# Kernel tuning notes

Hardware: AMD Instinct MI355X
Metric: run time of the kernel (lower is better)

Reference implementation:

```python
import jax, jax.numpy as jnp
import numpy as np

B, L, DM = 4, 1024, 1024
DI = int(2.0 * DM)            # d_inner = ssm_ratio * d_model
N = 16                        # d_state
R = int(np.ceil(DM / 16))     # dt_rank = 64
DT_MIN, DT_MAX = 1e-3, 1e-1


def setup_inputs() -> dict:
    key = jax.random.key(0)
    ks = jax.random.split(key, 8)
    s = 0.02
    # dt_proj bias init: inverse-softplus of log-uniform dt in [dt_min, dt_max]
    dt = jnp.exp(jax.random.uniform(ks[5], (DI,)) * (np.log(DT_MAX) - np.log(DT_MIN)) + np.log(DT_MIN))
    dt_bias = dt + jnp.log(-jnp.expm1(-dt))
    # A_log init: log(1..N) tiled per channel (S4D-real init)
    A_logs = jnp.log(jnp.tile(jnp.arange(1, N + 1, dtype=jnp.float32), (DI, 1)))
    return {
        "x": jax.random.normal(ks[0], (B, L, DM), jnp.float32),
        "W_in": jax.random.normal(ks[1], (DM, 2 * DI), jnp.float32) * s,
        "conv_w": jax.random.normal(ks[2], (DI, 1, 3), jnp.float32) * 0.1,
        "conv_b": jnp.zeros((DI,), jnp.float32),
        "W_x": jax.random.normal(ks[3], (DI, R + 2 * N), jnp.float32) * s,
        "W_dt": jax.random.normal(ks[4], (R, DI), jnp.float32) * (R ** -0.5),
        "dt_bias": dt_bias.astype(jnp.float32),
        "A_logs": A_logs,
        "Ds": jnp.ones((DI,), jnp.float32),
        "ln_g": jnp.ones((DI,), jnp.float32),
        "ln_b": jnp.zeros((DI,), jnp.float32),
        "W_out": jax.random.normal(ks[6], (DI, DM), jnp.float32) * s,
        "b_out": jnp.zeros((DM,), jnp.float32),
    }


def reference(x, W_in, conv_w, conv_b, W_x, W_dt, dt_bias, A_logs, Ds, ln_g, ln_b, W_out, b_out):
    di, n = Ds.shape[0], A_logs.shape[1]
    r = W_dt.shape[0]
    # in_proj and gate branch
    xz = x @ W_in                                   # (B,L,2*di)
    xi = xz[..., :di]
    z = jax.nn.silu(xz[..., di:])                   # (B,L,di)
    # depthwise conv over sequence dim (kernel 3, pad 1)
    xc = jnp.swapaxes(xi, 1, 2)                     # (B,di,L)
    xc = jax.lax.conv_general_dilated(
        xc, conv_w, (1,), [(1, 1)],
        dimension_numbers=("NCH", "OIH", "NCH"),
        feature_group_count=di) + conv_b[None, :, None]
    u = jax.nn.silu(jnp.swapaxes(xc, 1, 2))         # (B,L,di)
    # input-dependent dt, B, C
    x_dbl = u @ W_x                                 # (B,L,r+2n)
    dts = x_dbl[..., :r] @ W_dt                     # (B,L,di)
    Bs = x_dbl[..., r:r + n]                        # (B,L,n)
    Cs = x_dbl[..., r + n:]                         # (B,L,n)
    delta = jax.nn.softplus(dts + dt_bias)          # (B,L,di)
    A = -jnp.exp(A_logs)                            # (di,n)

    def step(h, inp):
        dt, ut, bt, ct = inp                        # (B,di),(B,di),(B,n),(B,n)
        h = jnp.exp(dt[..., None] * A) * h + (dt * ut)[..., None] * bt[:, None, :]
        return h, jnp.einsum("bdn,bn->bd", h, ct)

    xs = (jnp.swapaxes(delta, 0, 1), jnp.swapaxes(u, 0, 1),
          jnp.swapaxes(Bs, 0, 1), jnp.swapaxes(Cs, 0, 1))
    h0 = jnp.zeros((x.shape[0], di, n), x.dtype)
    _, ys = jax.lax.scan(step, h0, xs)              # (L,B,di)
    y = jnp.swapaxes(ys, 0, 1) + Ds * u             # skip term D*u
    # LayerNorm over channels
    mu = y.mean(-1, keepdims=True)
    var = ((y - mu) ** 2).mean(-1, keepdims=True)
    y = (y - mu) / jnp.sqrt(var + 1e-5) * ln_g + ln_b
    y = y * z                                       # gating
    v = y.mean(axis=1)                              # pool='mean' over D
    return v @ W_out + b_out                        # (B, out_dim)
```

## Files before the change

kernel.cpp:

```cpp
#include <hip/hip_runtime.h>
#include <math.h>

#define B_ 4
#define L_ 1024
#define DM_ 1024
#define DI_ 2048
#define N_ 16
#define R_ 64
#define BT_ (B_*L_)
#define NX_ 96
#define CH_ 16
#define LC_ (L_/CH_)
#define KC_ 8
#define KCL_ (DI_/KC_)

typedef unsigned short u16;
typedef unsigned int u32;
typedef short bf16x8 __attribute__((ext_vector_type(8)));
typedef u16 u16x8 __attribute__((ext_vector_type(8)));
typedef float f32x4 __attribute__((ext_vector_type(4)));

__device__ __forceinline__ float silu_f(float x) { return x / (1.f + expf(-x)); }
__device__ __forceinline__ float softplus_f(float x) {
  return x > 0.f ? x + log1pf(expf(-x)) : log1pf(expf(x));
}
__device__ __forceinline__ u16 bf16_rne(float f) {
  u32 u = __float_as_uint(f);
  u32 r = (u + 0x7FFFu + ((u >> 16) & 1u)) >> 16;
  return (u16)r;
}
__device__ __forceinline__ float bf16_to_f(u16 h) {
  return __uint_as_float(((u32)h) << 16);
}
__device__ __forceinline__ void gload_lds16(const void* g, void* l) {
  __builtin_amdgcn_global_load_lds((const __attribute__((address_space(1))) void*)g,
                                   (__attribute__((address_space(3))) void*)l, 16, 0, 0);
}

#define SWZ16(r, s) ((r) * 64 + ((((s) ^ (((r) >> 1) & 3))) << 4))

__global__ __launch_bounds__(256) void wsplit_kernel(const float* __restrict__ W,
                                                     u16* __restrict__ Th,
                                                     u16* __restrict__ Tl) {
  __shared__ float tile[32][33];
  const int n0 = blockIdx.x * 32;
  const int k0 = blockIdx.y * 32;
  const int t = threadIdx.x;
  {
    int kr = t >> 3, nc = (t & 7) * 4;
    float4 v = *(const float4*)&W[(size_t)(k0 + kr) * (2 * DI_) + n0 + nc];
    tile[kr][nc + 0] = v.x; tile[kr][nc + 1] = v.y;
    tile[kr][nc + 2] = v.z; tile[kr][nc + 3] = v.w;
  }
  __syncthreads();
  {
    int nr = t >> 3, kc = (t & 7) * 4;
    u16 h[4], l[4];
#pragma unroll
    for (int i = 0; i < 4; ++i) {
      float f = tile[kc + i][nr];
      h[i] = bf16_rne(f);
      l[i] = bf16_rne(f - bf16_to_f(h[i]));
    }
    size_t o = (size_t)(n0 + nr) * DM_ + k0 + kc;
    *(ushort4*)&Th[o] = make_ushort4(h[0], h[1], h[2], h[3]);
    *(ushort4*)&Tl[o] = make_ushort4(l[0], l[1], l[2], l[3]);
  }
}

__global__ __launch_bounds__(256) void xsplit_kernel(const float* __restrict__ x,
                                                     u16* __restrict__ xh,
                                                     u16* __restrict__ xl) {
  int gid = blockIdx.x * 256 + threadIdx.x;
  float4 v = *(const float4*)&x[(size_t)gid * 4];
  ushort4 h, l;
  h.x = bf16_rne(v.x); l.x = bf16_rne(v.x - bf16_to_f(h.x));
  h.y = bf16_rne(v.y); l.y = bf16_rne(v.y - bf16_to_f(h.y));
  h.z = bf16_rne(v.z); l.z = bf16_rne(v.z - bf16_to_f(h.z));
  h.w = bf16_rne(v.w); l.w = bf16_rne(v.w - bf16_to_f(h.w));
  *(ushort4*)&xh[(size_t)gid * 4] = h;
  *(ushort4*)&xl[(size_t)gid * 4] = l;
}

__global__ __launch_bounds__(512) void gemm1_mfma(const u16* __restrict__ Xh,
                                                  const u16* __restrict__ Xl,
                                                  const u16* __restrict__ Bh,
                                                  const u16* __restrict__ Bl,
                                                  float* __restrict__ xi,
                                                  float* __restrict__ z) {
  __shared__ __align__(16) char lds[49152];

  const int tid = threadIdx.x;
  const int m0 = blockIdx.x * 128;
  const int n0 = blockIdx.y * 256;
  const int wv = tid >> 6;
  const int lane = tid & 63;
  const int wr = wv >> 2, wc = wv & 3;
  const int lrow = lane & 15, lk = lane >> 4;

  const u16* gbase[6];
  int ldsO[6];
  size_t goff[6];
#pragma unroll
  for (int i = 0; i < 6; ++i) {
    int c = wv * 6 + i;
    int O = c << 10;
    int to;
    const u16* gb;
    if (O < 8192)       { gb = Xh + (size_t)m0 * DM_; to = O; }
    else if (O < 16384) { gb = Xl + (size_t)m0 * DM_; to = O - 8192; }
    else if (O < 32768) { gb = Bh + (size_t)n0 * DM_; to = O - 16384; }
    else                { gb = Bl + (size_t)n0 * DM_; to = O - 32768; }
    int r = (to >> 6) + (lane >> 2);
    int s_src = (lane & 3) ^ ((r >> 1) & 3);
    gbase[i] = gb;
    ldsO[i] = O;
    goff[i] = (size_t)r * DM_ + s_src * 8;
  }

  f32x4 acc[4][4];
#pragma unroll
  for (int i = 0; i < 4; ++i)
#pragma unroll
    for (int j = 0; j < 4; ++j) acc[i][j] = (f32x4){0.f, 0.f, 0.f, 0.f};

  for (int kk = 0; kk < DM_ / 32; ++kk) {
    const int k0 = kk * 32;
#pragma unroll
    for (int i = 0; i < 6; ++i) {
      gload_lds16(gbase[i] + goff[i] + k0, lds + ldsO[i]);
    }
    __syncthreads();

    bf16x8 a_h[4], a_l[4], b_h[4], b_l[4];
#pragma unroll
    for (int mi = 0; mi < 4; ++mi) {
      int r = wr * 64 + mi * 16 + lrow;
      a_h[mi] = *(const bf16x8*)(lds + SWZ16(r, lk));
      a_l[mi] = *(const bf16x8*)(lds + 8192 + SWZ16(r, lk));
    }
#pragma unroll
    for (int ni = 0; ni < 4; ++ni) {
      int r = wc * 64 + ni * 16 + lrow;
      b_h[ni] = *(const bf16x8*)(lds + 16384 + SWZ16(r, lk));
      b_l[ni] = *(const bf16x8*)(lds + 32768 + SWZ16(r, lk));
    }
#pragma unroll
    for (int mi = 0; mi < 4; ++mi)
#pragma unroll
      for (int ni = 0; ni < 4; ++ni) {
        acc[mi][ni] = __builtin_amdgcn_mfma_f32_16x16x32_bf16(a_h[mi], b_h[ni], acc[mi][ni], 0, 0, 0);
        acc[mi][ni] = __builtin_amdgcn_mfma_f32_16x16x32_bf16(a_h[mi], b_l[ni], acc[mi][ni], 0, 0, 0);
        acc[mi][ni] = __builtin_amdgcn_mfma_f32_16x16x32_bf16(a_l[mi], b_h[ni], acc[mi][ni], 0, 0, 0);
      }
    __syncthreads();
  }

  const bool is_z = (n0 >= DI_);
#pragma unroll
  for (int mi = 0; mi < 4; ++mi) {
#pragma unroll
    for (int ni = 0; ni < 4; ++ni) {
      int mrow = m0 + wr * 64 + mi * 16 + (lane >> 4) * 4;
      int ncol = n0 + wc * 64 + ni * 16 + (lane & 15);
#pragma unroll
      for (int rg = 0; rg < 4; ++rg) {
        float v = acc[mi][ni][rg];
        int m = mrow + rg;
        if (!is_z) {
          xi[(size_t)m * DI_ + ncol] = v;
        } else {
          z[(size_t)m * DI_ + (ncol - DI_)] = silu_f(v);
        }
      }
    }
  }
}

__global__ __launch_bounds__(256) void conv_silu_kernel(const float* __restrict__ xi,
                                                        const float* __restrict__ cw,
                                                        const float* __restrict__ cb,
                                                        float* __restrict__ u) {
  int gid = blockIdx.x * 256 + threadIdx.x;
  int idx = gid * 4;
  int d = idx & (DI_ - 1);
  int t = (idx >> 11) & (L_ - 1);
  float4 xc = *(const float4*)&xi[idx];
  float4 xm = make_float4(0.f, 0.f, 0.f, 0.f);
  float4 xp = make_float4(0.f, 0.f, 0.f, 0.f);
  if (t > 0) xm = *(const float4*)&xi[idx - DI_];
  if (t < L_ - 1) xp = *(const float4*)&xi[idx + DI_];
  float4 o;
  {
    float w0 = cw[(d + 0) * 3], w1 = cw[(d + 0) * 3 + 1], w2 = cw[(d + 0) * 3 + 2];
    o.x = silu_f(cb[d + 0] + w0 * xm.x + w1 * xc.x + w2 * xp.x);
  }
  {
    float w0 = cw[(d + 1) * 3], w1 = cw[(d + 1) * 3 + 1], w2 = cw[(d + 1) * 3 + 2];
    o.y = silu_f(cb[d + 1] + w0 * xm.y + w1 * xc.y + w2 * xp.y);
  }
  {
    float w0 = cw[(d + 2) * 3], w1 = cw[(d + 2) * 3 + 1], w2 = cw[(d + 2) * 3 + 2];
    o.z = silu_f(cb[d + 2] + w0 * xm.z + w1 * xc.z + w2 * xp.z);
  }
  {
    float w0 = cw[(d + 3) * 3], w1 = cw[(d + 3) * 3 + 1], w2 = cw[(d + 3) * 3 + 2];
    o.w = silu_f(cb[d + 3] + w0 * xm.w + w1 * xc.w + w2 * xp.w);
  }
  *(float4*)&u[idx] = o;
}

__global__ __launch_bounds__(256) void wxsplit_kernel(const float* __restrict__ Wx,
                                                      u16* __restrict__ Th,
                                                      u16* __restrict__ Tl) {
  int gid = blockIdx.x * 256 + threadIdx.x;
  int n = gid >> 11;
  int k = gid & (DI_ - 1);
  float f = Wx[(size_t)k * NX_ + n];
  u16 h = bf16_rne(f);
  Th[gid] = h;
  Tl[gid] = bf16_rne(f - bf16_to_f(h));
}

__global__ __launch_bounds__(256) void xdbl_mfma(const float* __restrict__ U,
                                                 const u16* __restrict__ Wh,
                                                 const u16* __restrict__ Wl,
                                                 float* __restrict__ Pt) {
  __shared__ u16 Uh_s[128 * 32];
  __shared__ u16 Ul_s[128 * 32];
  __shared__ u16 Wh_s[96 * 32];
  __shared__ u16 Wl_s[96 * 32];

  const int tid = threadIdx.x;
  const int m0 = blockIdx.x * 128;
  const int kc = blockIdx.y;
  const int wv = tid >> 6;
  const int lane = tid & 63;
  const int lrow = lane & 15, lk = lane >> 4;
  const int ra = tid >> 1;
  const int hf = tid & 1;

  f32x4 acc[2][6];
#pragma unroll
  for (int i = 0; i < 2; ++i)
#pragma unroll
    for (int j = 0; j < 6; ++j) acc[i][j] = (f32x4){0.f, 0.f, 0.f, 0.f};

  float af[16];
  uint4 wh_r[3], wl_r[3];
  int wc_row[3], wc_slot[3], wc_buf[3];

  {
    int k0 = kc * KCL_;
    const float* up = &U[(size_t)(m0 + ra) * DI_ + k0 + hf * 16];
    float4 a0 = *(const float4*)(up + 0);
    float4 a1 = *(const float4*)(up + 4);
    float4 a2 = *(const float4*)(up + 8);
    float4 a3 = *(const float4*)(up + 12);
    af[0]=a0.x; af[1]=a0.y; af[2]=a0.z; af[3]=a0.w;
    af[4]=a1.x; af[5]=a1.y; af[6]=a1.z; af[7]=a1.w;
    af[8]=a2.x; af[9]=a2.y; af[10]=a2.z; af[11]=a2.w;
    af[12]=a3.x; af[13]=a3.y; af[14]=a3.z; af[15]=a3.w;
#pragma unroll
    for (int i = 0; i < 3; ++i) {
      int c = tid + 256 * i;
      int buf = c >= 384;
      int cc = c & 383;
      int row = cc >> 2, slot = cc & 3;
      wc_buf[i] = buf; wc_row[i] = row; wc_slot[i] = slot;
      const u16* src = (buf ? Wl : Wh) + (size_t)row * DI_ + k0 + slot * 8;
      uint4 v = *(const uint4*)src;
      if (buf) wl_r[i] = v; else wh_r[i] = v;
    }
  }

  for (int kk = 0; kk < KCL_ / 32; ++kk) {
    __syncthreads();
    {
      u16x8 hv0, hv1, lv0, lv1;
#pragma unroll
      for (int i = 0; i < 8; ++i) {
        u16 h = bf16_rne(af[i]);
        hv0[i] = h;
        lv0[i] = bf16_rne(af[i] - bf16_to_f(h));
      }
#pragma unroll
      for (int i = 0; i < 8; ++i) {
        u16 h = bf16_rne(af[8 + i]);
        hv1[i] = h;
        lv1[i] = bf16_rne(af[8 + i] - bf16_to_f(h));
      }
      int s0 = hf * 2;
      *(u16x8*)((char*)Uh_s + SWZ16(ra, s0)) = hv0;
      *(u16x8*)((char*)Uh_s + SWZ16(ra, s0 + 1)) = hv1;
      *(u16x8*)((char*)Ul_s + SWZ16(ra, s0)) = lv0;
      *(u16x8*)((char*)Ul_s + SWZ16(ra, s0 + 1)) = lv1;
#pragma unroll
      for (int i = 0; i < 3; ++i) {
        char* dst = (char*)(wc_buf[i] ? Wl_s : Wh_s) + SWZ16(wc_row[i], wc_slot[i]);
        *(uint4*)dst = wc_buf[i] ? wl_r[i] : wh_r[i];
      }
    }
    __syncthreads();

    if (kk + 1 < KCL_ / 32) {
      int k0 = kc * KCL_ + (kk + 1) * 32;
      const float* up = &U[(size_t)(m0 + ra) * DI_ + k0 + hf * 16];
      float4 a0 = *(const float4*)(up + 0);
      float4 a1 = *(const float4*)(up + 4);
      float4 a2 = *(const float4*)(up + 8);
      float4 a3 = *(const float4*)(up + 12);
      af[0]=a0.x; af[1]=a0.y; af[2]=a0.z; af[3]=a0.w;
      af[4]=a1.x; af[5]=a1.y; af[6]=a1.z; af[7]=a1.w;
      af[8]=a2.x; af[9]=a2.y; af[10]=a2.z; af[11]=a2.w;
      af[12]=a3.x; af[13]=a3.y; af[14]=a3.z; af[15]=a3.w;
#pragma unroll
      for (int i = 0; i < 3; ++i) {
        const u16* src = (wc_buf[i] ? Wl : Wh) + (size_t)wc_row[i] * DI_ + k0 + wc_slot[i] * 8;
        uint4 v = *(const uint4*)src;
        if (wc_buf[i]) wl_r[i] = v; else wh_r[i] = v;
      }
    }

    bf16x8 a_h[2], a_l[2], b_h[6], b_l[6];
#pragma unroll
    for (int mi = 0; mi < 2; ++mi) {
      int r = wv * 32 + mi * 16 + lrow;
      a_h[mi] = *(const bf16x8*)((const char*)Uh_s + SWZ16(r, lk));
      a_l[mi] = *(const bf16x8*)((const char*)Ul_s + SWZ16(r, lk));
    }
#pragma unroll
    for (int ni = 0; ni < 6; ++ni) {
      int r = ni * 16 + lrow;
      b_h[ni] = *(const bf16x8*)((const char*)Wh_s + SWZ16(r, lk));
      b_l[ni] = *(const bf16x8*)((const char*)Wl_s + SWZ16(r, lk));
    }
#pragma unroll
    for (int mi = 0; mi < 2; ++mi)
#pragma unroll
      for (int ni = 0; ni < 6; ++ni) {
        acc[mi][ni] = __builtin_amdgcn_mfma_f32_16x16x32_bf16(a_h[mi], b_h[ni], acc[mi][ni], 0, 0, 0);
        acc[mi][ni] = __builtin_amdgcn_mfma_f32_16x16x32_bf16(a_h[mi], b_l[ni], acc[mi][ni], 0, 0, 0);
        acc[mi][ni] = __builtin_amdgcn_mfma_f32_16x16x32_bf16(a_l[mi], b_h[ni], acc[mi][ni], 0, 0, 0);
      }
  }

#pragma unroll
  for (int mi = 0; mi < 2; ++mi) {
#pragma unroll
    for (int ni = 0; ni < 6; ++ni) {
      int mrow = m0 + wv * 32 + mi * 16 + (lane >> 4) * 4;
      int ncol = ni * 16 + (lane & 15);
#pragma unroll
      for (int rg = 0; rg < 4; ++rg) {
        Pt[((size_t)kc * BT_ + mrow + rg) * NX_ + ncol] = acc[mi][ni][rg];
      }
    }
  }
}

__global__ __launch_bounds__(256) void xdbl_reduce(const float* __restrict__ Pt,
                                                   float* __restrict__ xdbl) {
  int gid = blockIdx.x * 256 + threadIdx.x;
  float s = 0.f;
#pragma unroll
  for (int kc = 0; kc < KC_; ++kc) s += Pt[(size_t)kc * BT_ * NX_ + gid];
  xdbl[gid] = s;
}

__global__ __launch_bounds__(256) void delta_kernel(const float* __restrict__ xdbl,
                                                    const float* __restrict__ Wdt,
                                                    const float* __restrict__ dtb,
                                                    float* __restrict__ delta) {
  __shared__ float xs[8][R_];
  const int m0 = blockIdx.x * 8;
  const int tid = threadIdx.x;
  for (int i = tid; i < 8 * R_; i += 256) {
    int mi = i >> 6, r = i & 63;
    xs[mi][r] = xdbl[(size_t)(m0 + mi) * NX_ + r];
  }
  __syncthreads();
  float acc[8][8];
#pragma unroll
  for (int mi = 0; mi < 8; ++mi)
#pragma unroll
    for (int j = 0; j < 8; ++j) acc[mi][j] = 0.f;

  for (int r = 0; r < R_; ++r) {
    float wd[8];
#pragma unroll
    for (int j = 0; j < 8; ++j) wd[j] = Wdt[(size_t)r * DI_ + tid + j * 256];
#pragma unroll
    for (int mi = 0; mi < 8; ++mi) {
      float xr = xs[mi][r];
#pragma unroll
      for (int j = 0; j < 8; ++j) acc[mi][j] += xr * wd[j];
    }
  }
#pragma unroll
  for (int j = 0; j < 8; ++j) {
    int d = tid + j * 256;
    float bias = dtb[d];
#pragma unroll
    for (int mi = 0; mi < 8; ++mi) {
      delta[(size_t)(m0 + mi) * DI_ + d] = softplus_f(acc[mi][j] + bias);
    }
  }
}

__global__ __launch_bounds__(256) void scanA_kernel(const float* __restrict__ delta,
                                                    const float* __restrict__ u,
                                                    const float* __restrict__ xdbl,
                                                    const float* __restrict__ A_logs,
                                                    float* __restrict__ P,
                                                    float* __restrict__ Q) {
  const int tid = threadIdx.x;
  const int q = tid & 3;
  const int chan = blockIdx.x * 64 + (tid >> 2);
  const int c = blockIdx.y;
  const int b = chan >> 11;
  const int d = chan & (DI_ - 1);
  float Ac[4];
#pragma unroll
  for (int j = 0; j < 4; ++j) Ac[j] = -expf(A_logs[d * N_ + q * 4 + j]);
  const size_t base = (size_t)b * L_ * DI_ + d;
  const float* xd = xdbl + (size_t)b * L_ * NX_;
  float h[4] = {0.f, 0.f, 0.f, 0.f};
  float pr[4] = {1.f, 1.f, 1.f, 1.f};
  const int t0 = c * LC_;
  for (int tt = 0; tt < LC_; ++tt) {
    int t = t0 + tt;
    float dt = delta[base + (size_t)t * DI_];
    float ut = u[base + (size_t)t * DI_];
    float4 Bt = *(const float4*)&xd[t * NX_ + R_ + q * 4];
    float du = dt * ut;
    float e0 = __expf(dt * Ac[0]), e1 = __expf(dt * Ac[1]);
    float e2 = __expf(dt * Ac[2]), e3 = __expf(dt * Ac[3]);
    h[0] = e0 * h[0] + du * Bt.x; pr[0] *= e0;
    h[1] = e1 * h[1] + du * Bt.y; pr[1] *= e1;
    h[2] = e2 * h[2] + du * Bt.z; pr[2] *= e2;
    h[3] = e3 * h[3] + du * Bt.w; pr[3] *= e3;
  }
  size_t idx = ((size_t)chan * CH_ + c) * N_ + q * 4;
  *(float4*)&P[idx] = make_float4(pr[0], pr[1], pr[2], pr[3]);
  *(float4*)&Q[idx] = make_float4(h[0], h[1], h[2], h[3]);
}

__global__ __launch_bounds__(256) void scanB_kernel(const float* __restrict__ P,
                                                    const float* __restrict__ Q,
                                                    float* __restrict__ H0) {
  int gid = blockIdx.x * 256 + threadIdx.x;
  int chan = gid >> 4;
  int n = gid & 15;
  float h = 0.f;
  for (int c = 0; c < CH_; ++c) {
    size_t idx = ((size_t)chan * CH_ + c) * N_ + n;
    H0[idx] = h;
    h = P[idx] * h + Q[idx];
  }
}

__global__ __launch_bounds__(256) void scanC_kernel(const float* __restrict__ delta,
                                                    float* uy,
                                                    const float* __restrict__ xdbl,
                                                    const float* __restrict__ A_logs,
                                                    const float* __restrict__ Ds,
                                                    const float* __restrict__ H0) {
  const int tid = threadIdx.x;
  const int q = tid & 3;
  const int chan = blockIdx.x * 64 + (tid >> 2);
  const int c = blockIdx.y;
  const int b = chan >> 11;
  const int d = chan & (DI_ - 1);
  float Ac[4];
#pragma unroll
  for (int j = 0; j < 4; ++j) Ac[j] = -expf(A_logs[d * N_ + q * 4 + j]);
  const float Dd = Ds[d];
  const size_t base = (size_t)b * L_ * DI_ + d;
  const float* dl = delta + base;
  float* ul = uy + base;
  const float* xd = xdbl + (size_t)b * L_ * NX_;
  float h[4];
  {
    float4 h0 = *(const float4*)&H0[((size_t)chan * CH_ + c) * N_ + q * 4];
    h[0] = h0.x; h[1] = h0.y; h[2] = h0.z; h[3] = h0.w;
  }
  const int t0 = c * LC_;
  for (int tt = 0; tt < LC_; ++tt) {
    int t = t0 + tt;
    float dt = dl[(size_t)t * DI_];
    float ut = ul[(size_t)t * DI_];
    float4 Bt = *(const float4*)&xd[t * NX_ + R_ + q * 4];
    float4 Ct = *(const float4*)&xd[t * NX_ + R_ + N_ + q * 4];
    float du = dt * ut;
    float e0 = __expf(dt * Ac[0]), e1 = __expf(dt * Ac[1]);
    float e2 = __expf(dt * Ac[2]), e3 = __expf(dt * Ac[3]);
    h[0] = e0 * h[0] + du * Bt.x;
    h[1] = e1 * h[1] + du * Bt.y;
    h[2] = e2 * h[2] + du * Bt.z;
    h[3] = e3 * h[3] + du * Bt.w;
    float p = h[0] * Ct.x + h[1] * Ct.y + h[2] * Ct.z + h[3] * Ct.w;
    p += __shfl_xor(p, 1);
    p += __shfl_xor(p, 2);
    if (q == 0) ul[(size_t)t * DI_] = p + Dd * ut;
  }
}

__global__ __launch_bounds__(256) void stats_kernel(const float* __restrict__ y,
                                                    float* __restrict__ mu,
                                                    float* __restrict__ rs) {
  __shared__ float red[4];
  const int row = blockIdx.x;
  const float* yr = y + (size_t)row * DI_;
  const int tid = threadIdx.x;
  float v[8];
  float s = 0.f;
#pragma unroll
  for (int j = 0; j < 8; ++j) { v[j] = yr[tid + j * 256]; s += v[j]; }
#pragma unroll
  for (int o = 1; o < 64; o <<= 1) s += __shfl_xor(s, o);
  if ((tid & 63) == 0) red[tid >> 6] = s;
  __syncthreads();
  float mu_v = (red[0] + red[1] + red[2] + red[3]) * (1.f / DI_);
  float q = 0.f;
#pragma unroll
  for (int j = 0; j < 8; ++j) { float dd = v[j] - mu_v; q += dd * dd; }
#pragma unroll
  for (int o = 1; o < 64; o <<= 1) q += __shfl_xor(q, o);
  __syncthreads();
  if ((tid & 63) == 0) red[tid >> 6] = q;
  __syncthreads();
  if (tid == 0) {
    float var = (red[0] + red[1] + red[2] + red[3]) * (1.f / DI_);
    mu[row] = mu_v;
    rs[row] = rsqrtf(var + 1e-5f);
  }
}

__global__ __launch_bounds__(256) void vacc_kernel(const float* __restrict__ y,
                                                   const float* __restrict__ z,
                                                   const float* __restrict__ mu,
                                                   const float* __restrict__ rs,
                                                   const float* __restrict__ g,
                                                   const float* __restrict__ bb,
                                                   float* __restrict__ v) {
  const int d = blockIdx.x * 256 + threadIdx.x;
  const int t0 = blockIdx.y * 64;
  const int b = blockIdx.z;
  const float gg = g[d], bbv = bb[d];
  float acc = 0.f;
  for (int tt = 0; tt < 64; ++tt) {
    int row = b * L_ + t0 + tt;
    float yv = y[(size_t)row * DI_ + d];
    float zv = z[(size_t)row * DI_ + d];
    acc += ((yv - mu[row]) * rs[row] * gg + bbv) * zv;
  }
  atomicAdd(&v[b * DI_ + d], acc * (1.f / L_));
}

__global__ __launch_bounds__(256) void outinit_kernel(const float* __restrict__ b_out,
                                                      float* __restrict__ out) {
  int i = blockIdx.x * 256 + threadIdx.x;
  out[i] = b_out[i & (DM_ - 1)];
}

__global__ __launch_bounds__(256) void outgemm_kernel(const float* __restrict__ v,
                                                      const float* __restrict__ Wout,
                                                      float* __restrict__ out) {
  const int m = blockIdx.x * 256 + threadIdx.x;
  const int d0 = blockIdx.y * 128;
  float a0 = 0.f, a1 = 0.f, a2 = 0.f, a3 = 0.f;
  for (int dd = 0; dd < 128; ++dd) {
    float w = Wout[(size_t)(d0 + dd) * DM_ + m];
    a0 += v[0 * DI_ + d0 + dd] * w;
    a1 += v[1 * DI_ + d0 + dd] * w;
    a2 += v[2 * DI_ + d0 + dd] * w;
    a3 += v[3 * DI_ + d0 + dd] * w;
  }
  atomicAdd(&out[0 * DM_ + m], a0);
  atomicAdd(&out[1 * DM_ + m], a1);
  atomicAdd(&out[2 * DM_ + m], a2);
  atomicAdd(&out[3 * DM_ + m], a3);
}

extern "C" void kernel_launch(void* const* d_in, const int* in_sizes, int n_in,
                              void* d_out, int out_size, void* d_ws, size_t ws_size,
                              hipStream_t stream) {
  const float* x      = (const float*)d_in[0];
  const float* W_in   = (const float*)d_in[1];
  const float* conv_w = (const float*)d_in[2];
  const float* conv_b = (const float*)d_in[3];
  const float* W_x    = (const float*)d_in[4];
  const float* W_dt   = (const float*)d_in[5];
  const float* dt_bias= (const float*)d_in[6];
  const float* A_logs = (const float*)d_in[7];
  const float* Ds     = (const float*)d_in[8];
  const float* ln_g   = (const float*)d_in[9];
  const float* ln_b   = (const float*)d_in[10];
  const float* W_out  = (const float*)d_in[11];
  const float* b_out  = (const float*)d_in[12];
  float* out = (float*)d_out;

  float* ws = (float*)d_ws;
  const size_t BIG = (size_t)BT_ * DI_;
  float* xi_buf   = ws;
  float* z_buf    = ws + BIG;
  float* u_buf    = ws + 2 * BIG;
  float* xdbl_buf = ws + 3 * BIG;
  float* mu_buf   = xdbl_buf + (size_t)BT_ * NX_;
  float* rs_buf   = mu_buf + BT_;
  float* v_buf    = rs_buf + BT_;
  float* P_buf    = v_buf + (size_t)B_ * DI_;
  float* Q_buf    = P_buf + (size_t)B_ * DI_ * CH_ * N_;
  float* H0_buf   = Q_buf + (size_t)B_ * DI_ * CH_ * N_;

  u16* wt_hi = (u16*)P_buf;
  u16* wt_lo = (u16*)Q_buf;
  u16* wx_hi = (u16*)H0_buf;
  u16* wx_lo = wx_hi + (size_t)NX_ * DI_;
  u16* xh = (u16*)u_buf;
  u16* xl = xh + (size_t)BT_ * DM_;
  float* xdbl_part = xi_buf;

  hipMemsetAsync(v_buf, 0, (size_t)B_ * DI_ * sizeof(float), stream);

  wsplit_kernel<<<dim3((2 * DI_) / 32, DM_ / 32), 256, 0, stream>>>(W_in, wt_hi, wt_lo);
  xsplit_kernel<<<(BT_ * DM_) / 1024, 256, 0, stream>>>(x, xh, xl);
  gemm1_mfma<<<dim3(BT_ / 128, (2 * DI_) / 256), 512, 0, stream>>>(xh, xl, wt_hi, wt_lo,
                                                                   xi_buf, z_buf);
  conv_silu_kernel<<<(BT_ * DI_) / 1024, 256, 0, stream>>>(xi_buf, conv_w, conv_b, u_buf);
  wxsplit_kernel<<<(NX_ * DI_) / 256, 256, 0, stream>>>(W_x, wx_hi, wx_lo);
  xdbl_mfma<<<dim3(BT_ / 128, KC_), 256, 0, stream>>>(u_buf, wx_hi, wx_lo, xdbl_part);
  xdbl_reduce<<<(BT_ * NX_) / 256, 256, 0, stream>>>(xdbl_part, xdbl_buf);
  delta_kernel<<<BT_ / 8, 256, 0, stream>>>(xdbl_buf, W_dt, dt_bias, xi_buf);
  scanA_kernel<<<dim3((B_ * DI_) / 64, CH_), 256, 0, stream>>>(xi_buf, u_buf, xdbl_buf,
                                                               A_logs, P_buf, Q_buf);
  scanB_kernel<<<(B_ * DI_ * N_) / 256, 256, 0, stream>>>(P_buf, Q_buf, H0_buf);
  scanC_kernel<<<dim3((B_ * DI_) / 64, CH_), 256, 0, stream>>>(xi_buf, u_buf, xdbl_buf,
                                                               A_logs, Ds, H0_buf);
  stats_kernel<<<BT_, 256, 0, stream>>>(u_buf, mu_buf, rs_buf);
  vacc_kernel<<<dim3(DI_ / 256, L_ / 64, B_), 256, 0, stream>>>(u_buf, z_buf, mu_buf, rs_buf,
                                                                ln_g, ln_b, v_buf);
  outinit_kernel<<<(B_ * DM_) / 256, 256, 0, stream>>>(b_out, out);
  outgemm_kernel<<<dim3(DM_ / 256, DI_ / 128), 256, 0, stream>>>(v_buf, W_out, out);
}
```

Baseline: 334.9 us.

## Fuse split-K reduce via atomics, fuse LN stats with pooling, simplify scan decay

Removes the xdbl partial-sum buffer and reduce kernel by having each split-K block atomically add into a zeroed xdbl. In the chunked scan, the product of per-step decays is replaced by one exponential of A times the summed dt. LayerNorm statistics and the gated mean pooling are merged into one per-row kernel that atomically accumulates every element into the pooled vector. This removes launches and intermediate traffic but adds heavy atomic contention on the pooled output and nondeterministic summation order.

```diff
diff --git a/kernel.cpp b/kernel.cpp
--- a/kernel.cpp
+++ b/kernel.cpp
@@ -225,7 +225,7 @@
 __global__ __launch_bounds__(256) void xdbl_mfma(const float* __restrict__ U,
                                                  const u16* __restrict__ Wh,
                                                  const u16* __restrict__ Wl,
-                                                 float* __restrict__ Pt) {
+                                                 float* __restrict__ xdbl) {
   __shared__ u16 Uh_s[128 * 32];
   __shared__ u16 Ul_s[128 * 32];
   __shared__ u16 Wh_s[96 * 32];
@@ -353,19 +353,10 @@
       int ncol = ni * 16 + (lane & 15);
 #pragma unroll
       for (int rg = 0; rg < 4; ++rg) {
-        Pt[((size_t)kc * BT_ + mrow + rg) * NX_ + ncol] = acc[mi][ni][rg];
-      }
-    }
-  }
-}
-
-__global__ __launch_bounds__(256) void xdbl_reduce(const float* __restrict__ Pt,
-                                                   float* __restrict__ xdbl) {
-  int gid = blockIdx.x * 256 + threadIdx.x;
-  float s = 0.f;
-#pragma unroll
-  for (int kc = 0; kc < KC_; ++kc) s += Pt[(size_t)kc * BT_ * NX_ + gid];
-  xdbl[gid] = s;
+        atomicAdd(&xdbl[(size_t)(mrow + rg) * NX_ + ncol], acc[mi][ni][rg]);
+      }
+    }
+  }
 }
 
 __global__ __launch_bounds__(256) void delta_kernel(const float* __restrict__ xdbl,
@@ -426,7 +417,7 @@
   const size_t base = (size_t)b * L_ * DI_ + d;
   const float* xd = xdbl + (size_t)b * L_ * NX_;
   float h[4] = {0.f, 0.f, 0.f, 0.f};
-  float pr[4] = {1.f, 1.f, 1.f, 1.f};
+  float sdt = 0.f;
   const int t0 = c * LC_;
   for (int tt = 0; tt < LC_; ++tt) {
     int t = t0 + tt;
@@ -436,13 +427,15 @@
     float du = dt * ut;
     float e0 = __expf(dt * Ac[0]), e1 = __expf(dt * Ac[1]);
     float e2 = __expf(dt * Ac[2]), e3 = __expf(dt * Ac[3]);
-    h[0] = e0 * h[0] + du * Bt.x; pr[0] *= e0;
-    h[1] = e1 * h[1] + du * Bt.y; pr[1] *= e1;
-    h[2] = e2 * h[2] + du * Bt.z; pr[2] *= e2;
-    h[3] = e3 * h[3] + du * Bt.w; pr[3] *= e3;
+    h[0] = e0 * h[0] + du * Bt.x;
+    h[1] = e1 * h[1] + du * Bt.y;
+    h[2] = e2 * h[2] + du * Bt.z;
+    h[3] = e3 * h[3] + du * Bt.w;
+    sdt += dt;
   }
   size_t idx = ((size_t)chan * CH_ + c) * N_ + q * 4;
-  *(float4*)&P[idx] = make_float4(pr[0], pr[1], pr[2], pr[3]);
+  *(float4*)&P[idx] = make_float4(__expf(Ac[0] * sdt), __expf(Ac[1] * sdt),
+                                  __expf(Ac[2] * sdt), __expf(Ac[3] * sdt));
   *(float4*)&Q[idx] = make_float4(h[0], h[1], h[2], h[3]);
 }
 
@@ -506,56 +499,41 @@
   }
 }
 
-__global__ __launch_bounds__(256) void stats_kernel(const float* __restrict__ y,
-                                                    float* __restrict__ mu,
-                                                    float* __restrict__ rs) {
+__global__ __launch_bounds__(256) void lnz_kernel(const float* __restrict__ y,
+                                                  const float* __restrict__ z,
+                                                  const float* __restrict__ g,
+                                                  const float* __restrict__ bb,
+                                                  float* __restrict__ v) {
   __shared__ float red[4];
   const int row = blockIdx.x;
+  const int b = row >> 10;
   const float* yr = y + (size_t)row * DI_;
+  const float* zr = z + (size_t)row * DI_;
   const int tid = threadIdx.x;
-  float v[8];
+  float vy[8];
   float s = 0.f;
 #pragma unroll
-  for (int j = 0; j < 8; ++j) { v[j] = yr[tid + j * 256]; s += v[j]; }
+  for (int j = 0; j < 8; ++j) { vy[j] = yr[tid + j * 256]; s += vy[j]; }
 #pragma unroll
   for (int o = 1; o < 64; o <<= 1) s += __shfl_xor(s, o);
   if ((tid & 63) == 0) red[tid >> 6] = s;
   __syncthreads();
   float mu_v = (red[0] + red[1] + red[2] + red[3]) * (1.f / DI_);
-  float q = 0.f;
-#pragma unroll
-  for (int j = 0; j < 8; ++j) { float dd = v[j] - mu_v; q += dd * dd; }
-#pragma unroll
-  for (int o = 1; o < 64; o <<= 1) q += __shfl_xor(q, o);
+  float qv = 0.f;
+#pragma unroll
+  for (int j = 0; j < 8; ++j) { float dd = vy[j] - mu_v; qv += dd * dd; }
+#pragma unroll
+  for (int o = 1; o < 64; o <<= 1) qv += __shfl_xor(qv, o);
   __syncthreads();
-  if ((tid & 63) == 0) red[tid >> 6] = q;
+  if ((tid & 63) == 0) red[tid >> 6] = qv;
   __syncthreads();
-  if (tid == 0) {
-    float var = (red[0] + red[1] + red[2] + red[3]) * (1.f / DI_);
-    mu[row] = mu_v;
-    rs[row] = rsqrtf(var + 1e-5f);
-  }
-}
-
-__global__ __launch_bounds__(256) void vacc_kernel(const float* __restrict__ y,
-                                                   const float* __restrict__ z,
-                                                   const float* __restrict__ mu,
-                                                   const float* __restrict__ rs,
-                                                   const float* __restrict__ g,
-                                                   const float* __restrict__ bb,
-                                                   float* __restrict__ v) {
-  const int d = blockIdx.x * 256 + threadIdx.x;
-  const int t0 = blockIdx.y * 64;
-  const int b = blockIdx.z;
-  const float gg = g[d], bbv = bb[d];
-  float acc = 0.f;
-  for (int tt = 0; tt < 64; ++tt) {
-    int row = b * L_ + t0 + tt;
-    float yv = y[(size_t)row * DI_ + d];
-    float zv = z[(size_t)row * DI_ + d];
-    acc += ((yv - mu[row]) * rs[row] * gg + bbv) * zv;
-  }
-  atomicAdd(&v[b * DI_ + d], acc * (1.f / L_));
+  float rs_v = rsqrtf((red[0] + red[1] + red[2] + red[3]) * (1.f / DI_) + 1e-5f);
+#pragma unroll
+  for (int j = 0; j < 8; ++j) {
+    int d = tid + j * 256;
+    float val = ((vy[j] - mu_v) * rs_v * g[d] + bb[d]) * zr[d];
+    atomicAdd(&v[b * DI_ + d], val * (1.f / L_));
+  }
 }
 
 __global__ __launch_bounds__(256) void outinit_kernel(const float* __restrict__ b_out,
@@ -607,9 +585,7 @@
   float* z_buf    = ws + BIG;
   float* u_buf    = ws + 2 * BIG;
   float* xdbl_buf = ws + 3 * BIG;
-  float* mu_buf   = xdbl_buf + (size_t)BT_ * NX_;
-  float* rs_buf   = mu_buf + BT_;
-  float* v_buf    = rs_buf + BT_;
+  float* v_buf    = xdbl_buf + (size_t)BT_ * NX_ + 2 * BT_;
   float* P_buf    = v_buf + (size_t)B_ * DI_;
   float* Q_buf    = P_buf + (size_t)B_ * DI_ * CH_ * N_;
   float* H0_buf   = Q_buf + (size_t)B_ * DI_ * CH_ * N_;
@@ -620,9 +596,9 @@
   u16* wx_lo = wx_hi + (size_t)NX_ * DI_;
   u16* xh = (u16*)u_buf;
   u16* xl = xh + (size_t)BT_ * DM_;
-  float* xdbl_part = xi_buf;
 
   hipMemsetAsync(v_buf, 0, (size_t)B_ * DI_ * sizeof(float), stream);
+  hipMemsetAsync(xdbl_buf, 0, (size_t)BT_ * NX_ * sizeof(float), stream);
 
   wsplit_kernel<<<dim3((2 * DI_) / 32, DM_ / 32), 256, 0, stream>>>(W_in, wt_hi, wt_lo);
   xsplit_kernel<<<(BT_ * DM_) / 1024, 256, 0, stream>>>(x, xh, xl);
@@ -630,17 +606,14 @@
                                                                    xi_buf, z_buf);
   conv_silu_kernel<<<(BT_ * DI_) / 1024, 256, 0, stream>>>(xi_buf, conv_w, conv_b, u_buf);
   wxsplit_kernel<<<(NX_ * DI_) / 256, 256, 0, stream>>>(W_x, wx_hi, wx_lo);
-  xdbl_mfma<<<dim3(BT_ / 128, KC_), 256, 0, stream>>>(u_buf, wx_hi, wx_lo, xdbl_part);
-  xdbl_reduce<<<(BT_ * NX_) / 256, 256, 0, stream>>>(xdbl_part, xdbl_buf);
+  xdbl_mfma<<<dim3(BT_ / 128, KC_), 256, 0, stream>>>(u_buf, wx_hi, wx_lo, xdbl_buf);
   delta_kernel<<<BT_ / 8, 256, 0, stream>>>(xdbl_buf, W_dt, dt_bias, xi_buf);
   scanA_kernel<<<dim3((B_ * DI_) / 64, CH_), 256, 0, stream>>>(xi_buf, u_buf, xdbl_buf,
                                                                A_logs, P_buf, Q_buf);
   scanB_kernel<<<(B_ * DI_ * N_) / 256, 256, 0, stream>>>(P_buf, Q_buf, H0_buf);
   scanC_kernel<<<dim3((B_ * DI_) / 64, CH_), 256, 0, stream>>>(xi_buf, u_buf, xdbl_buf,
                                                                A_logs, Ds, H0_buf);
-  stats_kernel<<<BT_, 256, 0, stream>>>(u_buf, mu_buf, rs_buf);
-  vacc_kernel<<<dim3(DI_ / 256, L_ / 64, B_), 256, 0, stream>>>(u_buf, z_buf, mu_buf, rs_buf,
-                                                                ln_g, ln_b, v_buf);
+  lnz_kernel<<<BT_, 256, 0, stream>>>(u_buf, z_buf, ln_g, ln_b, v_buf);
   outinit_kernel<<<(B_ * DM_) / 256, 256, 0, stream>>>(b_out, out);
   outgemm_kernel<<<dim3(DM_ / 256, DI_ / 128), 256, 0, stream>>>(v_buf, W_out, out);
 }
```

After: 393.9 us. 17.6% more time.
